# Performance work log

Measured on AMD Instinct MI355X. Metric: run time of the kernel, lower is better.

Reference implementation:

```python
import jax, jax.numpy as jnp
import numpy as np

EPS = 1e-6  # denominator stabilizer, matches eps=1e-6 default


def _feat(x):
    # elu_feature_map: elu(x) + 1 (positive feature map)
    return jax.nn.elu(x) + 1.0


def _causal_dot_product(Q, K, V):
    """Causal linear attention scan.
    Q, K: [N, L, H, E]; V: [N, L, H, M].
    Maintains running KV state S [N, H, E, M]; out_t = q_t . S_t.
    Equivalent to fast_transformers' causal_dot_product in O(N L H E M).
    """
    N, L, H, E = Q.shape
    M = V.shape[-1]

    def step(S, qkv):
        q, k, v = qkv  # [N,H,E], [N,H,E], [N,H,M]
        S = S + jnp.einsum('nhe,nhm->nhem', k, v)
        out = jnp.einsum('nhe,nhem->nhm', q, S)
        return S, out

    S0 = jnp.zeros((N, H, E, M), Q.dtype)
    qs = jnp.moveaxis(Q, 1, 0)  # [L,N,H,E]
    ks = jnp.moveaxis(K, 1, 0)
    vs = jnp.moveaxis(V, 1, 0)  # [L,N,H,M]
    _, out = jax.lax.scan(step, S0, (qs, ks, vs))  # out: [L,N,H,M]
    return jnp.moveaxis(out, 0, 1)  # [N,L,H,M]


def setup_inputs() -> dict:
    key = jax.random.key(0)
    k1, k2, k3 = jax.random.split(key, 3)
    N, L, H, E, M = 2, 8192, 8, 64, 64
    return {
        'queries': jax.random.normal(k1, (N, L, H, E), jnp.float32),
        'keys': jax.random.normal(k2, (N, L, H, E), jnp.float32),
        'values': jax.random.normal(k3, (N, L, H, M), jnp.float32),
        'key_mask': jnp.ones((N, L), jnp.float32),  # key_lengths.float_matrix
    }


def reference(queries, keys, values, key_mask):
    Q = _feat(queries)                                   # [N,L,H,E]
    K = _feat(keys) * key_mask[:, :, None, None]         # [N,S,H,E]
    # non-causal normalized branch (what the source returns as V)
    Z = 1.0 / (jnp.einsum('nlhd,nhd->nlh', Q, K.sum(axis=1)) + EPS)
    KV = jnp.einsum('nshd,nshm->nhmd', K, values)        # [N,H,M,E]
    V = jnp.einsum('nlhd,nhmd,nlh->nlhm', Q, KV, Z)      # [N,L,H,M]
    # causal branch (Zc / causal_dot_product path computed by the source)
    Zc = 1.0 / (jnp.einsum('nlhd,nlhd->nlh', Q, jnp.cumsum(K, axis=1)) + EPS)
    Vc = _causal_dot_product(Q, K, values) * Zc[:, :, :, None]
    return (V, Vc)
```

## Files before the change

### kernel.cpp

```cpp
#include <hip/hip_runtime.h>

#define NN 2
#define LL 8192
#define HH 8
#define EE 64
#define MM 64
#define TT 128
#define CC (LL/TT)
#define FEPS 1e-6f

typedef __attribute__((ext_vector_type(8)))  short short8;
typedef __attribute__((ext_vector_type(16))) float f32x16;

__device__ __forceinline__ float featf(float x) {
    return x > 0.f ? x + 1.f : __expf(x);
}

__device__ __forceinline__ unsigned short f2bf(float x) {
    union { float f; unsigned u; } v; v.f = x;
    unsigned r = v.u + 0x7FFF + ((v.u >> 16) & 1);
    return (unsigned short)(r >> 16);
}

__device__ __forceinline__ unsigned cvtpk(float lo, float hi) {
    unsigned r;
    asm volatile("v_cvt_pk_bf16_f32 %0, %1, %2" : "=v"(r) : "v"(lo), "v"(hi));
    return r;
}

__device__ __forceinline__ void plswap(unsigned &a, unsigned &b) {
    asm volatile("v_permlane32_swap_b32 %0, %1" : "+v"(a), "+v"(b));
}

#define ZERO16 {0.f,0.f,0.f,0.f,0.f,0.f,0.f,0.f,0.f,0.f,0.f,0.f,0.f,0.f,0.f,0.f}

#define KT_IDX(s,e) ((((s)*64)  + (e)) ^ (((s)&7)<<3))
#define VT_IDX(m,s) ((((m)*128) + (s)) ^ (((m)&7)<<3))
#define ST_IDX(m,e) ((((m)*64)  + (e)) ^ (((m)&7)<<3))

__global__ __launch_bounds__(256) void k_chunk_sums(
    const float* __restrict__ keys, const float* __restrict__ values,
    const float* __restrict__ mask,
    float* __restrict__ kv_chunk, float* __restrict__ ksum_chunk)
{
    __shared__ float kS[TT][EE];
    __shared__ float vS[TT][MM];

    const int b  = blockIdx.x;
    const int c  = b % CC;
    const int nh = b / CC;
    const int h  = nh % HH;
    const int n  = nh / HH;
    const int tid = threadIdx.x;

    const size_t rowstride = (size_t)HH * EE;
    const size_t base = ((size_t)(n*LL + c*TT) * HH + h) * EE;

    #pragma unroll
    for (int kk = 0; kk < 8; ++kk) {
        int j   = tid + kk*256;
        int row = j >> 4;
        int c4  = j & 15;
        float4 k4 = *(const float4*)(keys   + base + (size_t)row*rowstride + c4*4);
        float4 v4 = *(const float4*)(values + base + (size_t)row*rowstride + c4*4);
        float mv  = mask[n*LL + c*TT + row];
        float4 f;
        f.x = featf(k4.x)*mv; f.y = featf(k4.y)*mv;
        f.z = featf(k4.z)*mv; f.w = featf(k4.w)*mv;
        *(float4*)&kS[row][c4*4] = f;
        *(float4*)&vS[row][c4*4] = v4;
    }
    __syncthreads();

    const int e  = tid & 63;
    const int mq = tid >> 6;
    const int m0 = mq * 16;

    float acc[16];
    #pragma unroll
    for (int i = 0; i < 16; ++i) acc[i] = 0.f;

    for (int t = 0; t < TT; ++t) {
        float kv = kS[t][e];
        #pragma unroll
        for (int i4 = 0; i4 < 4; ++i4) {
            float4 v4 = *(const float4*)&vS[t][m0 + i4*4];
            acc[i4*4+0] += kv * v4.x;
            acc[i4*4+1] += kv * v4.y;
            acc[i4*4+2] += kv * v4.z;
            acc[i4*4+3] += kv * v4.w;
        }
    }

    float* dst = kv_chunk + (size_t)b*EE*MM + e*MM + m0;
    #pragma unroll
    for (int i4 = 0; i4 < 4; ++i4) {
        float4 o;
        o.x = acc[i4*4+0]; o.y = acc[i4*4+1];
        o.z = acc[i4*4+2]; o.w = acc[i4*4+3];
        *(float4*)(dst + i4*4) = o;
    }

    if (tid < EE) {
        float s = 0.f;
        for (int t = 0; t < TT; ++t) s += kS[t][tid];
        ksum_chunk[(size_t)b*EE + tid] = s;
    }
}

__global__ __launch_bounds__(256) void k_scan_kv(
    float* __restrict__ kv_chunk, float* __restrict__ kv_total)
{
    const int part = blockIdx.x & 15;
    const int nh   = blockIdx.x >> 4;
    const int i    = part*256 + threadIdx.x;

    float* bufb = kv_chunk + (size_t)nh*CC*EE*MM + i;

    float vals[CC];
    #pragma unroll
    for (int c = 0; c < CC; ++c) vals[c] = bufb[(size_t)c*EE*MM];

    float run = 0.f;
    #pragma unroll
    for (int c = 0; c < CC; ++c) {
        float v = vals[c];
        bufb[(size_t)c*EE*MM] = run;
        run += v;
    }
    kv_total[(size_t)nh*EE*MM + i] = run;
}

__global__ __launch_bounds__(64) void k_scan_ksum(
    float* __restrict__ ksum_chunk, float* __restrict__ ksum_total)
{
    const int nh = blockIdx.x;
    const int e  = threadIdx.x;
    float* bufb = ksum_chunk + (size_t)nh*CC*EE + e;

    float vals[CC];
    #pragma unroll
    for (int c = 0; c < CC; ++c) vals[c] = bufb[c*EE];

    float run = 0.f;
    #pragma unroll
    for (int c = 0; c < CC; ++c) {
        float v = vals[c];
        bufb[c*EE] = run;
        run += v;
    }
    ksum_total[nh*EE + e] = run;
}

__global__ __launch_bounds__(256) void k_output(
    const float* __restrict__ qin, const float* __restrict__ kin,
    const float* __restrict__ vin, const float* __restrict__ mask,
    const float* __restrict__ kv_prefix, const float* __restrict__ ksum_prefix,
    const float* __restrict__ kv_total,  const float* __restrict__ ksum_total,
    float* __restrict__ outV, float* __restrict__ outVc)
{
    __shared__ unsigned short kT[TT*EE];
    __shared__ unsigned short vT[MM*TT];
    __shared__ unsigned short sT[MM*EE];
    __shared__ unsigned short gT[MM*EE];
    __shared__ float kspS[EE];
    __shared__ float kstS[EE];

    const int b  = blockIdx.x;
    const int c  = b % CC;
    const int nh = b / CC;
    const int h  = nh % HH;
    const int n  = nh / HH;
    const int tid = threadIdx.x;

    const size_t rowstride = (size_t)HH * EE;
    const size_t base = ((size_t)(n*LL + c*TT) * HH + h) * EE;

    {
        const int s2   = tid >> 1;
        const int half = tid & 1;
        const float mv = mask[n*LL + c*TT + s2];
        const float* krow = kin + base + (size_t)s2*rowstride + half*32;
        const float* vrow = vin + base + (size_t)s2*rowstride + half*32;
        #pragma unroll
        for (int i = 0; i < 8; ++i) {
            float4 k4 = *(const float4*)(krow + i*4);
            int e0 = half*32 + i*4;
            unsigned short b0 = f2bf(featf(k4.x)*mv);
            unsigned short b1 = f2bf(featf(k4.y)*mv);
            unsigned short b2 = f2bf(featf(k4.z)*mv);
            unsigned short b3 = f2bf(featf(k4.w)*mv);
            uint2 wv; wv.x = (unsigned)b0 | ((unsigned)b1 << 16);
            wv.y = (unsigned)b2 | ((unsigned)b3 << 16);
            *(uint2*)&kT[KT_IDX(s2, e0)] = wv;
        }
        #pragma unroll
        for (int i = 0; i < 8; ++i) {
            float4 v4 = *(const float4*)(vrow + i*4);
            int m0 = half*32 + i*4;
            vT[VT_IDX(m0+0, s2)] = f2bf(v4.x);
            vT[VT_IDX(m0+1, s2)] = f2bf(v4.y);
            vT[VT_IDX(m0+2, s2)] = f2bf(v4.z);
            vT[VT_IDX(m0+3, s2)] = f2bf(v4.w);
        }
    }
    {
        const int e  = tid >> 2;
        const int m0 = (tid & 3) * 16;
        const float* sp = kv_prefix + (size_t)b*EE*MM  + (size_t)e*MM + m0;
        const float* gp = kv_total  + (size_t)nh*EE*MM + (size_t)e*MM + m0;
        #pragma unroll
        for (int i4 = 0; i4 < 4; ++i4) {
            float4 s4 = *(const float4*)(sp + i4*4);
            float4 g4 = *(const float4*)(gp + i4*4);
            int mb = m0 + i4*4;
            sT[ST_IDX(mb+0, e)] = f2bf(s4.x);  gT[ST_IDX(mb+0, e)] = f2bf(g4.x);
            sT[ST_IDX(mb+1, e)] = f2bf(s4.y);  gT[ST_IDX(mb+1, e)] = f2bf(g4.y);
            sT[ST_IDX(mb+2, e)] = f2bf(s4.z);  gT[ST_IDX(mb+2, e)] = f2bf(g4.z);
            sT[ST_IDX(mb+3, e)] = f2bf(s4.w);  gT[ST_IDX(mb+3, e)] = f2bf(g4.w);
        }
    }
    if (tid < EE) {
        kspS[tid] = ksum_prefix[(size_t)b*EE + tid];
        kstS[tid] = ksum_total[(size_t)nh*EE + tid];
    }
    __syncthreads();

    const int w    = tid >> 6;
    const int lane = tid & 63;
    const int rho  = lane & 31;
    const int hi   = lane >> 5;
    const int tch  = w + 4*rho;

    short8 qf[4];
    float zcI = 0.f, znI = 0.f;
    {
        const float* qrow = qin + base + (size_t)tch*rowstride;
        #pragma unroll
        for (int ks = 0; ks < 4; ++ks) {
            int e0 = ks*16 + hi*8;
            float4 a = *(const float4*)(qrow + e0);
            float4 d = *(const float4*)(qrow + e0 + 4);
            float qv0 = featf(a.x), qv1 = featf(a.y), qv2 = featf(a.z), qv3 = featf(a.w);
            float qv4 = featf(d.x), qv5 = featf(d.y), qv6 = featf(d.z), qv7 = featf(d.w);
            zcI += qv0*kspS[e0+0] + qv1*kspS[e0+1] + qv2*kspS[e0+2] + qv3*kspS[e0+3]
                 + qv4*kspS[e0+4] + qv5*kspS[e0+5] + qv6*kspS[e0+6] + qv7*kspS[e0+7];
            znI += qv0*kstS[e0+0] + qv1*kstS[e0+1] + qv2*kstS[e0+2] + qv3*kstS[e0+3]
                 + qv4*kstS[e0+4] + qv5*kstS[e0+5] + qv6*kstS[e0+6] + qv7*kstS[e0+7];
            short8 f;
            f[0] = (short)f2bf(qv0); f[1] = (short)f2bf(qv1);
            f[2] = (short)f2bf(qv2); f[3] = (short)f2bf(qv3);
            f[4] = (short)f2bf(qv4); f[5] = (short)f2bf(qv5);
            f[6] = (short)f2bf(qv6); f[7] = (short)f2bf(qv7);
            qf[ks] = f;
        }
    }

    f32x16 accC0 = ZERO16, accC1 = ZERO16, accN0 = ZERO16, accN1 = ZERO16;
    float zcs = 0.f;

    #pragma unroll
    for (int st = 0; st < 4; ++st) {
        short8 kf0 = *(const short8*)&kT[KT_IDX(st*32 + rho,  0 + hi*8)];
        short8 kf1 = *(const short8*)&kT[KT_IDX(st*32 + rho, 16 + hi*8)];
        short8 kf2 = *(const short8*)&kT[KT_IDX(st*32 + rho, 32 + hi*8)];
        short8 kf3 = *(const short8*)&kT[KT_IDX(st*32 + rho, 48 + hi*8)];

        f32x16 d = ZERO16;
        d = __builtin_amdgcn_mfma_f32_32x32x16_bf16(kf0, qf[0], d, 0, 0, 0);
        d = __builtin_amdgcn_mfma_f32_32x32x16_bf16(kf1, qf[1], d, 0, 0, 0);
        d = __builtin_amdgcn_mfma_f32_32x32x16_bf16(kf2, qf[2], d, 0, 0, 0);
        d = __builtin_amdgcn_mfma_f32_32x32x16_bf16(kf3, qf[3], d, 0, 0, 0);

        float pm[16];
        #pragma unroll
        for (int r = 0; r < 16; ++r) {
            int sl  = (r&3) + 8*(r>>2) + 4*hi;
            int sch = st*32 + sl;
            float vv = (sch <= tch) ? d[r] : 0.f;
            pm[r] = vv;
            zcs += vv;
        }

        unsigned c01 = cvtpk(pm[0],  pm[1]),  c23 = cvtpk(pm[2],  pm[3]);
        unsigned c45 = cvtpk(pm[4],  pm[5]),  c67 = cvtpk(pm[6],  pm[7]);
        plswap(c01, c45); plswap(c23, c67);
        unsigned c89 = cvtpk(pm[8],  pm[9]),  cab = cvtpk(pm[10], pm[11]);
        unsigned ccd = cvtpk(pm[12], pm[13]), cef = cvtpk(pm[14], pm[15]);
        plswap(c89, ccd); plswap(cab, cef);

        union { unsigned u[4]; short8 s; } uA, uB;
        uA.u[0] = c01; uA.u[1] = c23; uA.u[2] = c45; uA.u[3] = c67;
        uB.u[0] = c89; uB.u[1] = cab; uB.u[2] = ccd; uB.u[3] = cef;
        short8 paA = uA.s, paB = uB.s;

        {
            short8 v0 = *(const short8*)&vT[VT_IDX( 0 + rho, st*32 +  0 + hi*8)];
            short8 v1 = *(const short8*)&vT[VT_IDX( 0 + rho, st*32 + 16 + hi*8)];
            accC0 = __builtin_amdgcn_mfma_f32_32x32x16_bf16(paA, v0, accC0, 0, 0, 0);
            accC0 = __builtin_amdgcn_mfma_f32_32x32x16_bf16(paB, v1, accC0, 0, 0, 0);
        }
        {
            short8 v0 = *(const short8*)&vT[VT_IDX(32 + rho, st*32 +  0 + hi*8)];
            short8 v1 = *(const short8*)&vT[VT_IDX(32 + rho, st*32 + 16 + hi*8)];
            accC1 = __builtin_amdgcn_mfma_f32_32x32x16_bf16(paA, v0, accC1, 0, 0, 0);
            accC1 = __builtin_amdgcn_mfma_f32_32x32x16_bf16(paB, v1, accC1, 0, 0, 0);
        }
    }

    #pragma unroll
    for (int ks = 0; ks < 4; ++ks) {
        int e0 = ks*16 + hi*8;
        short8 sf0 = *(const short8*)&sT[ST_IDX( 0 + rho, e0)];
        short8 sf1 = *(const short8*)&sT[ST_IDX(32 + rho, e0)];
        short8 gf0 = *(const short8*)&gT[ST_IDX( 0 + rho, e0)];
        short8 gf1 = *(const short8*)&gT[ST_IDX(32 + rho, e0)];
        accC0 = __builtin_amdgcn_mfma_f32_32x32x16_bf16(qf[ks], sf0, accC0, 0, 0, 0);
        accC1 = __builtin_amdgcn_mfma_f32_32x32x16_bf16(qf[ks], sf1, accC1, 0, 0, 0);
        accN0 = __builtin_amdgcn_mfma_f32_32x32x16_bf16(qf[ks], gf0, accN0, 0, 0, 0);
        accN1 = __builtin_amdgcn_mfma_f32_32x32x16_bf16(qf[ks], gf1, accN1, 0, 0, 0);
    }

    float zc = zcs + zcI;
    zc += __shfl_xor(zc, 32, 64);
    float zn = znI;
    zn += __shfl_xor(zn, 32, 64);
    float zci = 1.f / (zc + FEPS);
    float zni = 1.f / (zn + FEPS);

    #pragma unroll
    for (int r = 0; r < 16; ++r) {
        int rrow = (r&3) + 8*(r>>2) + 4*hi;
        float zcr = __shfl(zci, rrow, 64);
        float znr = __shfl(zni, rrow, 64);
        int t = w + 4*rrow;
        size_t ob = ((size_t)(n*LL + c*TT + t)*HH + h)*MM;
        outVc[ob +      rho] = accC0[r] * zcr;
        outVc[ob + 32 + rho] = accC1[r] * zcr;
        outV [ob +      rho] = accN0[r] * znr;
        outV [ob + 32 + rho] = accN1[r] * znr;
    }
}

extern "C" void kernel_launch(void* const* d_in, const int* in_sizes, int n_in,
                              void* d_out, int out_size, void* d_ws, size_t ws_size,
                              hipStream_t stream) {
    const float* q    = (const float*)d_in[0];
    const float* k    = (const float*)d_in[1];
    const float* v    = (const float*)d_in[2];
    const float* mask = (const float*)d_in[3];

    float* outV  = (float*)d_out;
    float* outVc = outV + (size_t)NN*LL*HH*MM;

    float* kv_chunk   = (float*)d_ws;
    float* ksum_chunk = kv_chunk   + (size_t)NN*HH*CC*EE*MM;
    float* kv_total   = ksum_chunk + (size_t)NN*HH*CC*EE;
    float* ksum_total = kv_total   + (size_t)NN*HH*EE*MM;

    k_chunk_sums<<<NN*HH*CC, 256, 0, stream>>>(k, v, mask, kv_chunk, ksum_chunk);
    k_scan_kv  <<<NN*HH*16, 256, 0, stream>>>(kv_chunk, kv_total);
    k_scan_ksum<<<NN*HH,     64, 0, stream>>>(ksum_chunk, ksum_total);
    k_output   <<<NN*HH*CC, 256, 0, stream>>>(q, k, v, mask,
                                              kv_chunk, ksum_chunk,
                                              kv_total, ksum_total,
                                              outV, outVc);
}
```

Measured before the change: 197.9 us.

## Precompute bf16 swizzled K/V/S images and DMA them into LDS in output kernel

The chunk-sum kernel now converts masked feature K and V to bf16 swizzled tile images in global memory, computes per-chunk KV with MFMA instead of scalar FMAs, and stores KV transposed. The two scan kernels are merged into one that writes bf16 swizzled prefix and total state images. The output kernel then loads all four tiles with global_load_lds DMA instead of re-reading fp32 K/V and recomputing the feature map. This removes redundant fp32 reads and conversions in the output kernel and one launch, at the cost of extra workspace traffic and bf16 rounding of per-chunk KV and ksum.

Result: faster. 190.3 us (-3.9%).

```diff
diff --git a/kernel.cpp b/kernel.cpp
--- a/kernel.cpp
+++ b/kernel.cpp
@@ -22,6 +22,11 @@
     return (unsigned short)(r >> 16);
 }
 
+__device__ __forceinline__ float bf2f(unsigned short x) {
+    union { unsigned u; float f; } v; v.u = ((unsigned)x) << 16;
+    return v.f;
+}
+
 __device__ __forceinline__ unsigned cvtpk(float lo, float hi) {
     unsigned r;
     asm volatile("v_cvt_pk_bf16_f32 %0, %1, %2" : "=v"(r) : "v"(lo), "v"(hi));
@@ -32,19 +37,27 @@
     asm volatile("v_permlane32_swap_b32 %0, %1" : "+v"(a), "+v"(b));
 }
 
+__device__ __forceinline__ void dma16(const unsigned short* g, unsigned short* l) {
+    __builtin_amdgcn_global_load_lds(
+        (const __attribute__((address_space(1))) unsigned int*)(g),
+        (__attribute__((address_space(3))) unsigned int*)(l), 16, 0, 0);
+}
+
 #define ZERO16 {0.f,0.f,0.f,0.f,0.f,0.f,0.f,0.f,0.f,0.f,0.f,0.f,0.f,0.f,0.f,0.f}
 
-#define KT_IDX(s,e) ((((s)*64)  + (e)) ^ (((s)&7)<<3))
-#define VT_IDX(m,s) ((((m)*128) + (s)) ^ (((m)&7)<<3))
-#define ST_IDX(m,e) ((((m)*64)  + (e)) ^ (((m)&7)<<3))
+#define KT_IDX(s,e)  ((((s)*64)  + (e)) ^ (((s)&7)<<3))
+#define KTT_IDX(e,s) ((((e)*128) + (s)) ^ (((e)&7)<<3))
+#define VT_IDX(m,s)  ((((m)*128) + (s)) ^ (((m)&7)<<3))
+#define ST_IDX(m,e)  ((((m)*64)  + (e)) ^ (((m)&7)<<3))
 
 __global__ __launch_bounds__(256) void k_chunk_sums(
-    const float* __restrict__ keys, const float* __restrict__ values,
+    const float* __restrict__ kin, const float* __restrict__ vin,
     const float* __restrict__ mask,
-    float* __restrict__ kv_chunk, float* __restrict__ ksum_chunk)
+    unsigned short* __restrict__ Kimg, unsigned short* __restrict__ Vimg,
+    float* __restrict__ kv_chunkT, float* __restrict__ ksum_chunk)
 {
-    __shared__ float kS[TT][EE];
-    __shared__ float vS[TT][MM];
+    __shared__ unsigned short kTT[EE*TT];
+    __shared__ unsigned short vTl[MM*TT];
 
     const int b  = blockIdx.x;
     const int c  = b % CC;
@@ -56,107 +69,111 @@
     const size_t rowstride = (size_t)HH * EE;
     const size_t base = ((size_t)(n*LL + c*TT) * HH + h) * EE;
 
-    #pragma unroll
-    for (int kk = 0; kk < 8; ++kk) {
-        int j   = tid + kk*256;
-        int row = j >> 4;
-        int c4  = j & 15;
-        float4 k4 = *(const float4*)(keys   + base + (size_t)row*rowstride + c4*4);
-        float4 v4 = *(const float4*)(values + base + (size_t)row*rowstride + c4*4);
-        float mv  = mask[n*LL + c*TT + row];
-        float4 f;
-        f.x = featf(k4.x)*mv; f.y = featf(k4.y)*mv;
-        f.z = featf(k4.z)*mv; f.w = featf(k4.w)*mv;
-        *(float4*)&kS[row][c4*4] = f;
-        *(float4*)&vS[row][c4*4] = v4;
+    const int s2 = tid >> 1, half = tid & 1;
+    const float mv = mask[n*LL + c*TT + s2];
+    const float* krow = kin + base + (size_t)s2*rowstride + half*32;
+    const float* vrow = vin + base + (size_t)s2*rowstride + half*32;
+    unsigned short* kdst = Kimg + (size_t)b*(TT*EE);
+
+    #pragma unroll
+    for (int i = 0; i < 8; ++i) {
+        float4 k4 = *(const float4*)(krow + i*4);
+        int e0 = half*32 + i*4;
+        unsigned short b0 = f2bf(featf(k4.x)*mv), b1 = f2bf(featf(k4.y)*mv);
+        unsigned short b2 = f2bf(featf(k4.z)*mv), b3 = f2bf(featf(k4.w)*mv);
+        uint2 wv; wv.x = (unsigned)b0 | ((unsigned)b1 << 16);
+        wv.y = (unsigned)b2 | ((unsigned)b3 << 16);
+        *(uint2*)(kdst + KT_IDX(s2, e0)) = wv;
+        kTT[KTT_IDX(e0+0, s2)] = b0;
+        kTT[KTT_IDX(e0+1, s2)] = b1;
+        kTT[KTT_IDX(e0+2, s2)] = b2;
+        kTT[KTT_IDX(e0+3, s2)] = b3;
+    }
+    #pragma unroll
+    for (int i = 0; i < 8; ++i) {
+        float4 v4 = *(const float4*)(vrow + i*4);
+        int m0 = half*32 + i*4;
+        vTl[VT_IDX(m0+0, s2)] = f2bf(v4.x);
+        vTl[VT_IDX(m0+1, s2)] = f2bf(v4.y);
+        vTl[VT_IDX(m0+2, s2)] = f2bf(v4.z);
+        vTl[VT_IDX(m0+3, s2)] = f2bf(v4.w);
     }
     __syncthreads();
 
-    const int e  = tid & 63;
-    const int mq = tid >> 6;
-    const int m0 = mq * 16;
-
-    float acc[16];
-    #pragma unroll
-    for (int i = 0; i < 16; ++i) acc[i] = 0.f;
-
-    for (int t = 0; t < TT; ++t) {
-        float kv = kS[t][e];
-        #pragma unroll
-        for (int i4 = 0; i4 < 4; ++i4) {
-            float4 v4 = *(const float4*)&vS[t][m0 + i4*4];
-            acc[i4*4+0] += kv * v4.x;
-            acc[i4*4+1] += kv * v4.y;
-            acc[i4*4+2] += kv * v4.z;
-            acc[i4*4+3] += kv * v4.w;
-        }
-    }
-
-    float* dst = kv_chunk + (size_t)b*EE*MM + e*MM + m0;
-    #pragma unroll
-    for (int i4 = 0; i4 < 4; ++i4) {
-        float4 o;
-        o.x = acc[i4*4+0]; o.y = acc[i4*4+1];
-        o.z = acc[i4*4+2]; o.w = acc[i4*4+3];
-        *(float4*)(dst + i4*4) = o;
+    {
+        uint4* d = (uint4*)(Vimg + (size_t)b*(MM*TT));
+        const uint4* s = (const uint4*)vTl;
+        #pragma unroll
+        for (int j = 0; j < 4; ++j) d[tid + j*256] = s[tid + j*256];
+    }
+
+    const int w = tid >> 6, lane = tid & 63, rho = lane & 31, hi = lane >> 5;
+    const int mq = w >> 1, eq = w & 1;
+    f32x16 acc = ZERO16;
+    #pragma unroll
+    for (int ks = 0; ks < 8; ++ks) {
+        int t0 = ks*16 + hi*8;
+        short8 va = *(const short8*)&vTl[VT_IDX(mq*32 + rho, t0)];
+        short8 kb = *(const short8*)&kTT[KTT_IDX(eq*32 + rho, t0)];
+        acc = __builtin_amdgcn_mfma_f32_32x32x16_bf16(va, kb, acc, 0, 0, 0);
+    }
+    float* kvdst = kv_chunkT + (size_t)b*(EE*MM);
+    #pragma unroll
+    for (int r = 0; r < 16; ++r) {
+        int m = mq*32 + (r&3) + 8*(r>>2) + 4*hi;
+        kvdst[m*64 + eq*32 + rho] = acc[r];
     }
 
     if (tid < EE) {
         float s = 0.f;
-        for (int t = 0; t < TT; ++t) s += kS[t][tid];
+        #pragma unroll
+        for (int j = 0; j < 16; ++j) {
+            short8 kk8 = *(const short8*)&kTT[KTT_IDX(tid, j*8)];
+            #pragma unroll
+            for (int x = 0; x < 8; ++x) s += bf2f((unsigned short)kk8[x]);
+        }
         ksum_chunk[(size_t)b*EE + tid] = s;
     }
 }
 
-__global__ __launch_bounds__(256) void k_scan_kv(
-    float* __restrict__ kv_chunk, float* __restrict__ kv_total)
+__global__ __launch_bounds__(256) void k_scan(
+    const float* __restrict__ kv_chunkT, const float* __restrict__ ksum_chunk,
+    unsigned short* __restrict__ Simg, unsigned short* __restrict__ Gimg,
+    float* __restrict__ ksum_prefix, float* __restrict__ ksum_total)
 {
-    const int part = blockIdx.x & 15;
-    const int nh   = blockIdx.x >> 4;
-    const int i    = part*256 + threadIdx.x;
-
-    float* bufb = kv_chunk + (size_t)nh*CC*EE*MM + i;
-
+    const int part = blockIdx.x & 15, nh = blockIdx.x >> 4;
+    const int tid = threadIdx.x;
+    const int m = part*4 + (tid >> 6), e = tid & 63;
+
+    const float* src = kv_chunkT + (size_t)nh*CC*EE*MM + m*64 + e;
     float vals[CC];
     #pragma unroll
-    for (int c = 0; c < CC; ++c) vals[c] = bufb[(size_t)c*EE*MM];
-
+    for (int c = 0; c < CC; ++c) vals[c] = src[(size_t)c*EE*MM];
+
+    unsigned short* sdst = Simg + (size_t)nh*CC*EE*MM + ST_IDX(m, e);
     float run = 0.f;
     #pragma unroll
-    for (int c = 0; c < CC; ++c) {
-        float v = vals[c];
-        bufb[(size_t)c*EE*MM] = run;
-        run += v;
-    }
-    kv_total[(size_t)nh*EE*MM + i] = run;
-}
-
-__global__ __launch_bounds__(64) void k_scan_ksum(
-    float* __restrict__ ksum_chunk, float* __restrict__ ksum_total)
-{
-    const int nh = blockIdx.x;
-    const int e  = threadIdx.x;
-    float* bufb = ksum_chunk + (size_t)nh*CC*EE + e;
-
-    float vals[CC];
-    #pragma unroll
-    for (int c = 0; c < CC; ++c) vals[c] = bufb[c*EE];
-
-    float run = 0.f;
-    #pragma unroll
-    for (int c = 0; c < CC; ++c) {
-        float v = vals[c];
-        bufb[c*EE] = run;
-        run += v;
-    }
-    ksum_total[nh*EE + e] = run;
+    for (int c = 0; c < CC; ++c) { sdst[(size_t)c*EE*MM] = f2bf(run); run += vals[c]; }
+    Gimg[(size_t)nh*EE*MM + ST_IDX(m, e)] = f2bf(run);
+
+    if (part == 0 && tid < EE) {
+        const float* ks = ksum_chunk + (size_t)nh*CC*EE + tid;
+        float kv[CC];
+        #pragma unroll
+        for (int c = 0; c < CC; ++c) kv[c] = ks[c*EE];
+        float r2 = 0.f;
+        float* kp = ksum_prefix + (size_t)nh*CC*EE + tid;
+        #pragma unroll
+        for (int c = 0; c < CC; ++c) { kp[c*EE] = r2; r2 += kv[c]; }
+        ksum_total[nh*EE + tid] = r2;
+    }
 }
 
 __global__ __launch_bounds__(256) void k_output(
-    const float* __restrict__ qin, const float* __restrict__ kin,
-    const float* __restrict__ vin, const float* __restrict__ mask,
-    const float* __restrict__ kv_prefix, const float* __restrict__ ksum_prefix,
-    const float* __restrict__ kv_total,  const float* __restrict__ ksum_total,
+    const float* __restrict__ qin,
+    const unsigned short* __restrict__ Kimg, const unsigned short* __restrict__ Vimg,
+    const unsigned short* __restrict__ Simg, const unsigned short* __restrict__ Gimg,
+    const float* __restrict__ ksum_prefix,  const float* __restrict__ ksum_total,
     float* __restrict__ outV, float* __restrict__ outVc)
 {
     __shared__ unsigned short kT[TT*EE];
@@ -177,47 +194,20 @@
     const size_t base = ((size_t)(n*LL + c*TT) * HH + h) * EE;
 
     {
-        const int s2   = tid >> 1;
-        const int half = tid & 1;
-        const float mv = mask[n*LL + c*TT + s2];
-        const float* krow = kin + base + (size_t)s2*rowstride + half*32;
-        const float* vrow = vin + base + (size_t)s2*rowstride + half*32;
-        #pragma unroll
-        for (int i = 0; i < 8; ++i) {
-            float4 k4 = *(const float4*)(krow + i*4);
-            int e0 = half*32 + i*4;
-            unsigned short b0 = f2bf(featf(k4.x)*mv);
-            unsigned short b1 = f2bf(featf(k4.y)*mv);
-            unsigned short b2 = f2bf(featf(k4.z)*mv);
-            unsigned short b3 = f2bf(featf(k4.w)*mv);
-            uint2 wv; wv.x = (unsigned)b0 | ((unsigned)b1 << 16);
-            wv.y = (unsigned)b2 | ((unsigned)b3 << 16);
-            *(uint2*)&kT[KT_IDX(s2, e0)] = wv;
-        }
-        #pragma unroll
-        for (int i = 0; i < 8; ++i) {
-            float4 v4 = *(const float4*)(vrow + i*4);
-            int m0 = half*32 + i*4;
-            vT[VT_IDX(m0+0, s2)] = f2bf(v4.x);
-            vT[VT_IDX(m0+1, s2)] = f2bf(v4.y);
-            vT[VT_IDX(m0+2, s2)] = f2bf(v4.z);
-            vT[VT_IDX(m0+3, s2)] = f2bf(v4.w);
-        }
-    }
-    {
-        const int e  = tid >> 2;
-        const int m0 = (tid & 3) * 16;
-        const float* sp = kv_prefix + (size_t)b*EE*MM  + (size_t)e*MM + m0;
-        const float* gp = kv_total  + (size_t)nh*EE*MM + (size_t)e*MM + m0;
-        #pragma unroll
-        for (int i4 = 0; i4 < 4; ++i4) {
-            float4 s4 = *(const float4*)(sp + i4*4);
-            float4 g4 = *(const float4*)(gp + i4*4);
-            int mb = m0 + i4*4;
-            sT[ST_IDX(mb+0, e)] = f2bf(s4.x);  gT[ST_IDX(mb+0, e)] = f2bf(g4.x);
-            sT[ST_IDX(mb+1, e)] = f2bf(s4.y);  gT[ST_IDX(mb+1, e)] = f2bf(g4.y);
-            sT[ST_IDX(mb+2, e)] = f2bf(s4.z);  gT[ST_IDX(mb+2, e)] = f2bf(g4.z);
-            sT[ST_IDX(mb+3, e)] = f2bf(s4.w);  gT[ST_IDX(mb+3, e)] = f2bf(g4.w);
+        const unsigned short* kimg = Kimg + (size_t)b*(TT*EE);
+        const unsigned short* vimg = Vimg + (size_t)b*(MM*TT);
+        const unsigned short* simg = Simg + (size_t)b*(EE*MM);
+        const unsigned short* gimg = Gimg + (size_t)nh*(EE*MM);
+        const int wid = tid >> 6, ln = tid & 63;
+        #pragma unroll
+        for (int kk = 0; kk < 4; ++kk) {
+            dma16(kimg + (wid*4+kk)*512 + ln*8, &kT[(wid*4+kk)*512]);
+            dma16(vimg + (wid*4+kk)*512 + ln*8, &vT[(wid*4+kk)*512]);
+        }
+        #pragma unroll
+        for (int kk = 0; kk < 2; ++kk) {
+            dma16(simg + (wid*2+kk)*512 + ln*8, &sT[(wid*2+kk)*512]);
+            dma16(gimg + (wid*2+kk)*512 + ln*8, &gT[(wid*2+kk)*512]);
         }
     }
     if (tid < EE) {
@@ -353,16 +343,21 @@
     float* outV  = (float*)d_out;
     float* outVc = outV + (size_t)NN*LL*HH*MM;
 
-    float* kv_chunk   = (float*)d_ws;
-    float* ksum_chunk = kv_chunk   + (size_t)NN*HH*CC*EE*MM;
-    float* kv_total   = ksum_chunk + (size_t)NN*HH*CC*EE;
-    float* ksum_total = kv_total   + (size_t)NN*HH*EE*MM;
-
-    k_chunk_sums<<<NN*HH*CC, 256, 0, stream>>>(k, v, mask, kv_chunk, ksum_chunk);
-    k_scan_kv  <<<NN*HH*16, 256, 0, stream>>>(kv_chunk, kv_total);
-    k_scan_ksum<<<NN*HH,     64, 0, stream>>>(ksum_chunk, ksum_total);
-    k_output   <<<NN*HH*CC, 256, 0, stream>>>(q, k, v, mask,
-                                              kv_chunk, ksum_chunk,
-                                              kv_total, ksum_total,
-                                              outV, outVc);
-}
+    char* ws = (char*)d_ws;
+    float*          kv_chunkT   = (float*)(ws);
+    unsigned short* Kimg        = (unsigned short*)(ws + 16777216);
+    unsigned short* Vimg        = (unsigned short*)(ws + 33554432);
+    unsigned short* Simg        = (unsigned short*)(ws + 50331648);
+    unsigned short* Gimg        = (unsigned short*)(ws + 58720256);
+    float*          ksum_chunk  = (float*)(ws + 58851328);
+    float*          ksum_prefix = (float*)(ws + 59113472);
+    float*          ksum_total  = (float*)(ws + 59375616);
+
+    k_chunk_sums<<<NN*HH*CC, 256, 0, stream>>>(k, v, mask, Kimg, Vimg,
+                                               kv_chunkT, ksum_chunk);
+    k_scan      <<<NN*HH*16, 256, 0, stream>>>(kv_chunkT, ksum_chunk,
+                                               Simg, Gimg, ksum_prefix, ksum_total);
+    k_output    <<<NN*HH*CC, 256, 0, stream>>>(q, Kimg, Vimg, Simg, Gimg,
+                                               ksum_prefix, ksum_total,
+                                               outV, outVc);
+}
```
